# Optimization experiments

Hardware: AMD Instinct MI355X
Metric: run time of the kernel (lower is better)

## Reference

```python
import jax, jax.numpy as jnp
import numpy as np

N_NODES, N_EDGES = 100000, 1000000
NODE_IN, EDGE_IN, D_MODEL = 128, 64, 128


def setup_inputs() -> dict:
    key = jax.random.key(0)
    k1, k2, k3, k4, k5 = jax.random.split(key, 5)
    x_node = jax.random.normal(k1, (N_NODES, NODE_IN), dtype=jnp.float32)
    x_edge = jax.random.normal(k2, (N_EDGES, EDGE_IN), dtype=jnp.float32)
    edge_index = jax.random.randint(k3, (2, N_EDGES), 0, N_NODES, dtype=jnp.int64)
    # learned params (PyTorch Linear: y = x @ W.T + b)
    s_e = 1.0 / np.sqrt(EDGE_IN)
    s_n = 1.0 / np.sqrt(NODE_IN)
    W_edge = jax.random.uniform(k4, (D_MODEL, EDGE_IN), jnp.float32, -s_e, s_e)
    b_edge = jnp.zeros((D_MODEL,), jnp.float32)
    W_node = jax.random.uniform(k5, (D_MODEL, NODE_IN), jnp.float32, -s_n, s_n)
    b_node = jnp.zeros((D_MODEL,), jnp.float32)
    ln_gamma = jnp.ones((D_MODEL,), jnp.float32)
    ln_beta = jnp.zeros((D_MODEL,), jnp.float32)
    return {
        "x_node": x_node, "x_edge": x_edge, "edge_index": edge_index,
        "W_edge": W_edge, "b_edge": b_edge,
        "W_node": W_node, "b_node": b_node,
        "ln_gamma": ln_gamma, "ln_beta": ln_beta,
    }


def _layernorm(x, gamma, beta, eps=1e-5):
    mu = jnp.mean(x, axis=-1, keepdims=True)
    var = jnp.mean(jnp.square(x - mu), axis=-1, keepdims=True)
    return (x - mu) * jax.lax.rsqrt(var + eps) * gamma + beta


def reference(x_node, x_edge, edge_index, W_edge, b_edge, W_node, b_node, ln_gamma, ln_beta):
    src, dst = edge_index[0], edge_index[1]
    h_edge = x_edge @ W_edge.T + b_edge                       # [E, D]
    h_node = x_node @ W_node.T + b_node                       # [N, D] project once, then gather
    h_endpoints = (h_node[src] + h_node[dst]) * 0.5           # [E, D]
    return _layernorm(h_edge + h_endpoints, ln_gamma, ln_beta)
```

## Files before the change

kernel.cpp:

```cpp
#include <hip/hip_runtime.h>


typedef __attribute__((ext_vector_type(8))) short bf16x8;
typedef __attribute__((ext_vector_type(4))) float f32x4;

__device__ __forceinline__ short f2bf(float f) {
  unsigned u = __float_as_uint(f);
  u = (u + 0x7FFFu + ((u >> 16) & 1u)) >> 16;
  return (short)u;
}
__device__ __forceinline__ float bf2f(short s) {
  return __uint_as_float(((unsigned)(unsigned short)s) << 16);
}
__device__ __forceinline__ bf16x8 cvt8(const float* __restrict__ p) {
  const f32x4 a = *(const f32x4*)p;
  const f32x4 b = *(const f32x4*)(p + 4);
  bf16x8 r;
  r[0] = f2bf(a[0]); r[1] = f2bf(a[1]); r[2] = f2bf(a[2]); r[3] = f2bf(a[3]);
  r[4] = f2bf(b[0]); r[5] = f2bf(b[1]); r[6] = f2bf(b[2]); r[7] = f2bf(b[3]);
  return r;
}

__global__ __launch_bounds__(256) void node_mfma_kernel(
    const float* __restrict__ x_node,
    const float* __restrict__ W_node,
    const float* __restrict__ b_node,
    short* __restrict__ h_node,
    int n_nodes)
{
  __shared__ short Wlds[16384];
  __shared__ float blds[128];

  const int tid = threadIdx.x;
  {
    const int r = tid >> 1, h = tid & 1;
    const float* wr = W_node + (size_t)r * 128 + 64 * h;
#pragma unroll
    for (int q = 0; q < 8; ++q) {
      const bf16x8 v = cvt8(wr + 8 * q);
      const int slot = (8 * h + q) ^ (r & 7);
      *(bf16x8*)(&Wlds[r * 128 + slot * 8]) = v;
    }
    if (tid < 128) blds[tid] = b_node[tid];
  }
  __syncthreads();

  const int lane = tid & 63;
  const int c = lane & 15, g = lane >> 4;
  const int gw = blockIdx.x * 4 + (tid >> 6);
  const int nw = gridDim.x * 4;
  const int ntiles = (n_nodes + 15) >> 4;

  int woff[4];
#pragma unroll
  for (int s = 0; s < 4; ++s) woff[s] = c * 128 + ((4 * s + g) ^ (c & 7)) * 8;

  for (int tile = gw; tile < ntiles; tile += nw) {
    const int n0 = tile << 4;
    const int n = (n0 + c < n_nodes) ? n0 + c : n_nodes - 1;
    const float* xr = x_node + (size_t)n * 128;
    bf16x8 bx[4];
#pragma unroll
    for (int s = 0; s < 4; ++s) bx[s] = cvt8(xr + 32 * s + 8 * g);

    f32x4 acc[8];
#pragma unroll
    for (int t = 0; t < 8; ++t)
      acc[t] = *(const f32x4*)(blds + 16 * t + 4 * g);
#pragma unroll
    for (int t = 0; t < 8; ++t)
#pragma unroll
      for (int s = 0; s < 4; ++s) {
        const bf16x8 a = *(const bf16x8*)(&Wlds[t * 2048 + woff[s]]);
        acc[t] = __builtin_amdgcn_mfma_f32_16x16x32_bf16(a, bx[s], acc[t], 0, 0, 0);
      }

    if (n0 + c < n_nodes) {
      short* o = h_node + (size_t)(n0 + c) * 128 + g * 8;
#pragma unroll
      for (int k = 0; k < 4; ++k) {
        bf16x8 v;
#pragma unroll
        for (int j = 0; j < 4; ++j) {
          v[j]     = f2bf(acc[2 * k][j]);
          v[4 + j] = f2bf(acc[2 * k + 1][j]);
        }
        *(bf16x8*)(o + 32 * k) = v;
      }
    }
  }
}

__global__ __launch_bounds__(256) void edge_mfma_kernel(
    const float* __restrict__ x_edge,
    const int*   __restrict__ eidx,
    const float* __restrict__ W_edge,
    const float* __restrict__ b_edge,
    const short* __restrict__ h_node,
    const float* __restrict__ gamma,
    const float* __restrict__ beta,
    float* __restrict__ out,
    int n_edges)
{
  __shared__ short Wlds[8192];
  __shared__ float plds[384];

  const int tid = threadIdx.x;
  {
    const int r = tid >> 1, h = tid & 1;
    const float* wr = W_edge + (size_t)r * 64 + 32 * h;
#pragma unroll
    for (int q = 0; q < 4; ++q) {
      const bf16x8 v = cvt8(wr + 8 * q);
      const int slot = (4 * h + q) ^ (r & 7);
      *(bf16x8*)(&Wlds[r * 64 + slot * 8]) = v;
    }
    if (tid < 128) {
      plds[tid]       = b_edge[tid];
      plds[128 + tid] = gamma[tid];
      plds[256 + tid] = beta[tid];
    }
  }
  __syncthreads();

  const int lane = tid & 63;
  const int c = lane & 15, g = lane >> 4;
  const int gw = blockIdx.x * 4 + (tid >> 6);
  const int nw = gridDim.x * 4;
  const int ntiles = (n_edges + 15) >> 4;

  const int w0off = c * 64 + ((g) ^ (c & 7)) * 8;
  const int w1off = c * 64 + ((4 + g) ^ (c & 7)) * 8;

  if (gw >= ntiles) return;

  auto LOADIDX = [&](int tile, int& src, int& dst) {
    const int e = (tile * 16 + c < n_edges) ? tile * 16 + c : n_edges - 1;
    src = eidx[e];
    dst = eidx[n_edges + e];
  };
  auto LOADX = [&](int tile, bf16x8& b0, bf16x8& b1) {
    const int e = (tile * 16 + c < n_edges) ? tile * 16 + c : n_edges - 1;
    const float* xr = x_edge + (size_t)e * 64;
    b0 = cvt8(xr + 8 * g);
    b1 = cvt8(xr + 32 + 8 * g);
  };
  auto GATHER = [&](int src, int dst, bf16x8* vs, bf16x8* vd) {
    const short* hs = h_node + (size_t)src * 128 + g * 8;
    const short* hd = h_node + (size_t)dst * 128 + g * 8;
#pragma unroll
    for (int k = 0; k < 4; ++k) {
      vs[k] = *(const bf16x8*)(hs + 32 * k);
      vd[k] = *(const bf16x8*)(hd + 32 * k);
    }
  };

  bf16x8 bx0, bx1, bxN0, bxN1;
  bf16x8 vs[4], vd[4];
  int srcN, dstN;

  {
    int src0, dst0;
    LOADIDX(gw, src0, dst0);
    LOADX(gw, bx0, bx1);
    GATHER(src0, dst0, vs, vd);
    LOADIDX(gw + nw, srcN, dstN);
  }

  for (int t = gw; t < ntiles; t += nw) {
    f32x4 acc[8];
#pragma unroll
    for (int k = 0; k < 4; ++k)
#pragma unroll
      for (int j = 0; j < 4; ++j) {
        acc[2 * k][j]     = plds[16 * (2 * k) + 4 * g + j]
                          + 0.5f * (bf2f(vs[k][j]) + bf2f(vd[k][j]));
        acc[2 * k + 1][j] = plds[16 * (2 * k + 1) + 4 * g + j]
                          + 0.5f * (bf2f(vs[k][4 + j]) + bf2f(vd[k][4 + j]));
      }

    GATHER(srcN, dstN, vs, vd);
    LOADIDX(t + 2 * nw, srcN, dstN);
    LOADX(t + nw, bxN0, bxN1);

#pragma unroll
    for (int tt = 0; tt < 8; ++tt) {
      const bf16x8 a0 = *(const bf16x8*)(&Wlds[tt * 1024 + w0off]);
      const bf16x8 a1 = *(const bf16x8*)(&Wlds[tt * 1024 + w1off]);
      acc[tt] = __builtin_amdgcn_mfma_f32_16x16x32_bf16(a0, bx0, acc[tt], 0, 0, 0);
      acc[tt] = __builtin_amdgcn_mfma_f32_16x16x32_bf16(a1, bx1, acc[tt], 0, 0, 0);
    }

    float s1 = 0.f;
#pragma unroll
    for (int tt = 0; tt < 8; ++tt)
      s1 += (acc[tt][0] + acc[tt][1]) + (acc[tt][2] + acc[tt][3]);
    s1 += __shfl_xor(s1, 16, 64);
    s1 += __shfl_xor(s1, 32, 64);
    const float mu = s1 * (1.f / 128.f);

    float s2 = 0.f;
#pragma unroll
    for (int tt = 0; tt < 8; ++tt)
#pragma unroll
      for (int j = 0; j < 4; ++j) {
        const float d = acc[tt][j] - mu;
        acc[tt][j] = d;
        s2 = fmaf(d, d, s2);
      }
    s2 += __shfl_xor(s2, 16, 64);
    s2 += __shfl_xor(s2, 32, 64);
    const float rstd = rsqrtf(s2 * (1.f / 128.f) + 1e-5f);

    if (t * 16 + c < n_edges) {
      float* o = out + (size_t)(t * 16 + c) * 128 + 4 * g;
#pragma unroll
      for (int tt = 0; tt < 8; ++tt) {
        f32x4 r;
#pragma unroll
        for (int j = 0; j < 4; ++j)
          r[j] = fmaf(acc[tt][j] * rstd, plds[128 + 16 * tt + 4 * g + j],
                      plds[256 + 16 * tt + 4 * g + j]);
        *(f32x4*)(o + 16 * tt) = r;
      }
    }

    bx0 = bxN0; bx1 = bxN1;
  }
}

extern "C" void kernel_launch(void* const* d_in, const int* in_sizes, int n_in,
                              void* d_out, int out_size, void* d_ws, size_t ws_size,
                              hipStream_t stream) {
  const float* x_node = (const float*)d_in[0];
  const float* x_edge = (const float*)d_in[1];
  const int*   eidx   = (const int*)  d_in[2];
  const float* W_edge = (const float*)d_in[3];
  const float* b_edge = (const float*)d_in[4];
  const float* W_node = (const float*)d_in[5];
  const float* b_node = (const float*)d_in[6];
  const float* gamma  = (const float*)d_in[7];
  const float* beta   = (const float*)d_in[8];
  float* out = (float*)d_out;

  const int n_nodes = in_sizes[0] / 128;
  const int n_edges = in_sizes[2] / 2;

  short* h_node = (short*)d_ws;
  if (ws_size < (size_t)n_nodes * 128 * sizeof(short)) return;

  node_mfma_kernel<<<512, 256, 0, stream>>>(x_node, W_node, b_node, h_node, n_nodes);
  edge_mfma_kernel<<<2048, 256, 0, stream>>>(x_edge, eidx, W_edge, b_edge,
                                             h_node, gamma, beta, out, n_edges);
}
```

Before: 246.5 us.

## Replace node projection kernel with bf16 cast and per-edge recomputed node matmul

Drops the separate node projection kernel. A simple kernel now casts x_node to bf16, and the edge kernel gathers the raw src and dst node features and multiplies them by a 0.5-scaled W_node held in LDS. The node and edge biases are folded into a single bias. This removes the projected-node intermediate and one GEMM pass over the nodes. In exchange it multiplies the node-projection MFMA work by roughly the edge-to-node ratio and raises LDS use per block, which may lower occupancy in what was a bandwidth-bound edge kernel.

```diff
diff --git a/kernel.cpp b/kernel.cpp
--- a/kernel.cpp
+++ b/kernel.cpp
@@ -20,103 +20,62 @@
   r[4] = f2bf(b[0]); r[5] = f2bf(b[1]); r[6] = f2bf(b[2]); r[7] = f2bf(b[3]);
   return r;
 }
-
-__global__ __launch_bounds__(256) void node_mfma_kernel(
-    const float* __restrict__ x_node,
-    const float* __restrict__ W_node,
-    const float* __restrict__ b_node,
-    short* __restrict__ h_node,
-    int n_nodes)
+__device__ __forceinline__ bf16x8 cvt8s(const float* __restrict__ p, float sc) {
+  const f32x4 a = *(const f32x4*)p;
+  const f32x4 b = *(const f32x4*)(p + 4);
+  bf16x8 r;
+  r[0] = f2bf(sc * a[0]); r[1] = f2bf(sc * a[1]);
+  r[2] = f2bf(sc * a[2]); r[3] = f2bf(sc * a[3]);
+  r[4] = f2bf(sc * b[0]); r[5] = f2bf(sc * b[1]);
+  r[6] = f2bf(sc * b[2]); r[7] = f2bf(sc * b[3]);
+  return r;
+}
+
+__global__ __launch_bounds__(256) void cast_node_kernel(
+    const float* __restrict__ x, short* __restrict__ y, int nchunks)
 {
-  __shared__ short Wlds[16384];
-  __shared__ float blds[128];
-
-  const int tid = threadIdx.x;
-  {
-    const int r = tid >> 1, h = tid & 1;
-    const float* wr = W_node + (size_t)r * 128 + 64 * h;
-#pragma unroll
-    for (int q = 0; q < 8; ++q) {
-      const bf16x8 v = cvt8(wr + 8 * q);
-      const int slot = (8 * h + q) ^ (r & 7);
-      *(bf16x8*)(&Wlds[r * 128 + slot * 8]) = v;
-    }
-    if (tid < 128) blds[tid] = b_node[tid];
-  }
-  __syncthreads();
-
-  const int lane = tid & 63;
-  const int c = lane & 15, g = lane >> 4;
-  const int gw = blockIdx.x * 4 + (tid >> 6);
-  const int nw = gridDim.x * 4;
-  const int ntiles = (n_nodes + 15) >> 4;
-
-  int woff[4];
-#pragma unroll
-  for (int s = 0; s < 4; ++s) woff[s] = c * 128 + ((4 * s + g) ^ (c & 7)) * 8;
-
-  for (int tile = gw; tile < ntiles; tile += nw) {
-    const int n0 = tile << 4;
-    const int n = (n0 + c < n_nodes) ? n0 + c : n_nodes - 1;
-    const float* xr = x_node + (size_t)n * 128;
-    bf16x8 bx[4];
-#pragma unroll
-    for (int s = 0; s < 4; ++s) bx[s] = cvt8(xr + 32 * s + 8 * g);
-
-    f32x4 acc[8];
-#pragma unroll
-    for (int t = 0; t < 8; ++t)
-      acc[t] = *(const f32x4*)(blds + 16 * t + 4 * g);
-#pragma unroll
-    for (int t = 0; t < 8; ++t)
-#pragma unroll
-      for (int s = 0; s < 4; ++s) {
-        const bf16x8 a = *(const bf16x8*)(&Wlds[t * 2048 + woff[s]]);
-        acc[t] = __builtin_amdgcn_mfma_f32_16x16x32_bf16(a, bx[s], acc[t], 0, 0, 0);
-      }
-
-    if (n0 + c < n_nodes) {
-      short* o = h_node + (size_t)(n0 + c) * 128 + g * 8;
-#pragma unroll
-      for (int k = 0; k < 4; ++k) {
-        bf16x8 v;
-#pragma unroll
-        for (int j = 0; j < 4; ++j) {
-          v[j]     = f2bf(acc[2 * k][j]);
-          v[4 + j] = f2bf(acc[2 * k + 1][j]);
-        }
-        *(bf16x8*)(o + 32 * k) = v;
-      }
-    }
-  }
-}
-
-__global__ __launch_bounds__(256) void edge_mfma_kernel(
+  int i = blockIdx.x * 256 + threadIdx.x;
+  const int stride = gridDim.x * 256;
+  for (; i < nchunks; i += stride)
+    *(bf16x8*)(y + (size_t)i * 8) = cvt8(x + (size_t)i * 8);
+}
+
+__global__ __launch_bounds__(256) void edge_merged_kernel(
     const float* __restrict__ x_edge,
     const int*   __restrict__ eidx,
     const float* __restrict__ W_edge,
     const float* __restrict__ b_edge,
-    const short* __restrict__ h_node,
+    const float* __restrict__ W_node,
+    const float* __restrict__ b_node,
+    const short* __restrict__ xnb,
     const float* __restrict__ gamma,
     const float* __restrict__ beta,
     float* __restrict__ out,
     int n_edges)
 {
-  __shared__ short Wlds[8192];
+  __shared__ short Wn[16384];
+  __shared__ short We[8192];
   __shared__ float plds[384];
 
   const int tid = threadIdx.x;
   {
     const int r = tid >> 1, h = tid & 1;
-    const float* wr = W_edge + (size_t)r * 64 + 32 * h;
+    const float* we = W_edge + (size_t)r * 64 + 32 * h;
 #pragma unroll
     for (int q = 0; q < 4; ++q) {
-      const bf16x8 v = cvt8(wr + 8 * q);
+      const bf16x8 v = cvt8(we + 8 * q);
       const int slot = (4 * h + q) ^ (r & 7);
-      *(bf16x8*)(&Wlds[r * 64 + slot * 8]) = v;
+      *(bf16x8*)(&We[r * 64 + slot * 8]) = v;
+    }
+    const float* wn = W_node + (size_t)r * 128 + 64 * h;
+#pragma unroll
+    for (int q = 0; q < 8; ++q) {
+      const bf16x8 v = cvt8s(wn + 8 * q, 0.5f);
+      const int slot = (8 * h + q) ^ (r & 7);
+      *(bf16x8*)(&Wn[r * 128 + slot * 8]) = v;
     }
     if (tid < 128) {
-      plds[tid]       = b_edge[tid];
+      plds[tid]       = b_edge[tid] + b_node[tid];
       plds[128 + tid] = gamma[tid];
       plds[256 + tid] = beta[tid];
     }
@@ -129,8 +88,11 @@
   const int nw = gridDim.x * 4;
   const int ntiles = (n_edges + 15) >> 4;
 
-  const int w0off = c * 64 + ((g) ^ (c & 7)) * 8;
-  const int w1off = c * 64 + ((4 + g) ^ (c & 7)) * 8;
+  const int we0 = c * 64 + ((g) ^ (c & 7)) * 8;
+  const int we1 = c * 64 + ((4 + g) ^ (c & 7)) * 8;
+  int wn_off[4];
+#pragma unroll
+  for (int s = 0; s < 4; ++s) wn_off[s] = c * 128 + ((4 * s + g) ^ (c & 7)) * 8;
 
   if (gw >= ntiles) return;
 
@@ -145,48 +107,56 @@
     b0 = cvt8(xr + 8 * g);
     b1 = cvt8(xr + 32 + 8 * g);
   };
-  auto GATHER = [&](int src, int dst, bf16x8* vs, bf16x8* vd) {
-    const short* hs = h_node + (size_t)src * 128 + g * 8;
-    const short* hd = h_node + (size_t)dst * 128 + g * 8;
-#pragma unroll
-    for (int k = 0; k < 4; ++k) {
-      vs[k] = *(const bf16x8*)(hs + 32 * k);
-      vd[k] = *(const bf16x8*)(hd + 32 * k);
+  auto GATHER = [&](int src, int dst, bf16x8* xs, bf16x8* xd) {
+    const short* ps = xnb + (size_t)src * 128 + g * 8;
+    const short* pd = xnb + (size_t)dst * 128 + g * 8;
+#pragma unroll
+    for (int s = 0; s < 4; ++s) {
+      xs[s] = *(const bf16x8*)(ps + 32 * s);
+      xd[s] = *(const bf16x8*)(pd + 32 * s);
     }
   };
 
   bf16x8 bx0, bx1, bxN0, bxN1;
-  bf16x8 vs[4], vd[4];
+  bf16x8 xs[4], xd[4];
   int srcN, dstN;
 
   {
     int src0, dst0;
     LOADIDX(gw, src0, dst0);
     LOADX(gw, bx0, bx1);
-    GATHER(src0, dst0, vs, vd);
+    GATHER(src0, dst0, xs, xd);
     LOADIDX(gw + nw, srcN, dstN);
   }
 
   for (int t = gw; t < ntiles; t += nw) {
     f32x4 acc[8];
 #pragma unroll
-    for (int k = 0; k < 4; ++k)
-#pragma unroll
-      for (int j = 0; j < 4; ++j) {
-        acc[2 * k][j]     = plds[16 * (2 * k) + 4 * g + j]
-                          + 0.5f * (bf2f(vs[k][j]) + bf2f(vd[k][j]));
-        acc[2 * k + 1][j] = plds[16 * (2 * k + 1) + 4 * g + j]
-                          + 0.5f * (bf2f(vs[k][4 + j]) + bf2f(vd[k][4 + j]));
-      }
-
-    GATHER(srcN, dstN, vs, vd);
+    for (int tt = 0; tt < 8; ++tt)
+      acc[tt] = *(const f32x4*)(plds + 16 * tt + 4 * g);
+
+#pragma unroll
+    for (int s = 0; s < 4; ++s) {
+      bf16x8 a[8];
+#pragma unroll
+      for (int tt = 0; tt < 8; ++tt)
+        a[tt] = *(const bf16x8*)(&Wn[tt * 2048 + wn_off[s]]);
+#pragma unroll
+      for (int tt = 0; tt < 8; ++tt)
+        acc[tt] = __builtin_amdgcn_mfma_f32_16x16x32_bf16(a[tt], xs[s], acc[tt], 0, 0, 0);
+#pragma unroll
+      for (int tt = 0; tt < 8; ++tt)
+        acc[tt] = __builtin_amdgcn_mfma_f32_16x16x32_bf16(a[tt], xd[s], acc[tt], 0, 0, 0);
+    }
+
+    GATHER(srcN, dstN, xs, xd);
     LOADIDX(t + 2 * nw, srcN, dstN);
     LOADX(t + nw, bxN0, bxN1);
 
 #pragma unroll
     for (int tt = 0; tt < 8; ++tt) {
-      const bf16x8 a0 = *(const bf16x8*)(&Wlds[tt * 1024 + w0off]);
-      const bf16x8 a1 = *(const bf16x8*)(&Wlds[tt * 1024 + w1off]);
+      const bf16x8 a0 = *(const bf16x8*)(&We[tt * 1024 + we0]);
+      const bf16x8 a1 = *(const bf16x8*)(&We[tt * 1024 + we1]);
       acc[tt] = __builtin_amdgcn_mfma_f32_16x16x32_bf16(a0, bx0, acc[tt], 0, 0, 0);
       acc[tt] = __builtin_amdgcn_mfma_f32_16x16x32_bf16(a1, bx1, acc[tt], 0, 0, 0);
     }
@@ -246,10 +216,12 @@
   const int n_nodes = in_sizes[0] / 128;
   const int n_edges = in_sizes[2] / 2;
 
-  short* h_node = (short*)d_ws;
+  short* xnb = (short*)d_ws;
   if (ws_size < (size_t)n_nodes * 128 * sizeof(short)) return;
 
-  node_mfma_kernel<<<512, 256, 0, stream>>>(x_node, W_node, b_node, h_node, n_nodes);
-  edge_mfma_kernel<<<2048, 256, 0, stream>>>(x_edge, eidx, W_edge, b_edge,
-                                             h_node, gamma, beta, out, n_edges);
-}
+  const int nchunks = n_nodes * 16;
+  cast_node_kernel<<<2048, 256, 0, stream>>>(x_node, xnb, nchunks);
+  edge_merged_kernel<<<2048, 256, 0, stream>>>(x_edge, eidx, W_edge, b_edge,
+                                               W_node, b_node, xnb,
+                                               gamma, beta, out, n_edges);
+}
```

New measurement: 272.8 us. 10.7% more time.
